# Performance work log

Measured on AMD Instinct MI355X. Metric: run time of the kernel, lower is better.

Reference implementation:

```python
import jax, jax.numpy as jnp
import numpy as np

B, T, D, H, W = 2, 16, 64, 64, 64
MAX_GROWTH = 0.0  # max_growth_rate init kwarg

def _ln(x, g, b):
    m = x.mean(-1, keepdims=True)
    v = x.var(-1, keepdims=True)
    return (x - m) * jax.lax.rsqrt(v + 1e-5) * g + b

def _pscan(A, X):
    # linear recurrence h_t = A_t*h_{t-1} + X_t via Blelchlo-style associative scan over axis 1
    def comb(l, r):
        a1, x1 = l
        a2, x2 = r
        return a1 * a2, a2 * x1 + x2
    return jax.lax.associative_scan(comb, (A, X), axis=1)[1]

def setup_inputs() -> dict:
    key = jax.random.key(0)
    ks = jax.random.split(key, 20)
    n = lambda k, s, sc=1.0: jax.random.normal(k, s, dtype=jnp.float32) * sc
    inp = dict(
        x_re=n(ks[0], (B, T, D, H, W)), x_im=n(ks[1], (B, T, D, H, W)),
        h_re=n(ks[2], (B * H * W, 1, D)), h_im=n(ks[3], (B * H * W, 1, D)),
        flux_re=n(ks[4], (B, D)), flux_im=n(ks[5], (B, D)),
        dt_seq=0.01 + 0.1 * jax.random.uniform(ks[6], (B, T), dtype=jnp.float32),
        g_s=jnp.ones(2 * D, jnp.float32), b_s=jnp.zeros(2 * D, jnp.float32),
        Wc=n(ks[7], (3, 3, 2 * D, 2 * D), 1.0 / np.sqrt(9 * 2 * D)), bc=jnp.zeros(2 * D, jnp.float32),
        g_t=jnp.ones(2 * D, jnp.float32), b_t=jnp.zeros(2 * D, jnp.float32),
        E_re=n(ks[8], (D, D), 1.0 / np.sqrt(D)), E_im=n(ks[9], (D, D), 1.0 / np.sqrt(D)),
        Dec_re=n(ks[10], (D, D), 1.0 / np.sqrt(D)), Dec_im=n(ks[11], (D, D), 1.0 / np.sqrt(D)),
        lam_flux_raw=jnp.zeros(D, jnp.float32),
        Wsrc_re=n(ks[12], (D, D), 1.0 / np.sqrt(D)), Wsrc_im=n(ks[13], (D, D), 1.0 / np.sqrt(D)),
        w_gate=n(ks[14], (D,)), b_gate=jnp.zeros(D, jnp.float32),
        lam_re_raw=jnp.ones(D, jnp.float32), lam_im=n(ks[15], (D,)),
        W1=n(ks[16], (2 * D, 8 * D), 1.0 / np.sqrt(2 * D)), b1=jnp.zeros(8 * D, jnp.float32),
        W2=n(ks[17], (8 * D, 2 * D), 1.0 / np.sqrt(8 * D)), b2=jnp.zeros(2 * D, jnp.float32),
    )
    return inp

def _forward(x_re, x_im, h_re, h_im, flux_re, flux_im, dt_seq, g_s, b_s, Wc, bc, g_t, b_t,
             E_re, E_im, Dec_re, Dec_im, lam_flux_raw, Wsrc_re, Wsrc_im, w_gate, b_gate,
             lam_re_raw, lam_im, W1, b1, W2, b2):
    # channel-last complex field (B,T,H,W,D)
    x = jnp.moveaxis(x_re, 2, -1) + 1j * jnp.moveaxis(x_im, 2, -1)
    # --- spatial residual branch: LN -> Clifford(= real 2D conv on [re;im] channels) ---
    xr = jnp.concatenate([x.real, x.imag], -1)  # (B,T,H,W,2D)
    xn = _ln(xr, g_s, b_s).reshape(B * T, H, W, 2 * D)
    xs = jax.lax.conv_general_dilated(xn, Wc, (1, 1), 'SAME',
                                      dimension_numbers=('NHWC', 'HWIO', 'NHWC')) + bc
    xs = xs.reshape(B, T, H, W, 2 * D)
    x = x + (xs[..., :D] + 1j * xs[..., D:])
    # --- eigen-basis encode ---
    x_eig = jnp.einsum('bthwd,de->bthwe', x, E_re + 1j * E_im)
    x_mean = x_eig.mean((2, 3))  # (B,T,D)
    # --- flux tracker scan ---
    lam_f = jax.nn.softplus(lam_flux_raw)
    A_flux = jnp.exp(-lam_f * dt_seq[..., None])  # (B,T,D) real decay
    flux = _pscan(A_flux.astype(x_mean.dtype), x_mean * dt_seq[..., None])
    flux = flux + (flux_re + 1j * flux_im)[:, None, :] * jnp.cumprod(A_flux, axis=1)
    source = jnp.einsum('btd,de->bte', flux, Wsrc_re + 1j * Wsrc_im)
    gate = jax.nn.sigmoid(flux.real * w_gate + b_gate)  # real gate in [0,1]
    flux_out = flux[:, -1]
    ge = gate[:, :, None, None, :]
    forcing = x_eig * ge + source[:, :, None, None, :] * (1.0 - ge)
    # --- temporal propagator (exact exponential integrator) ---
    lam = (MAX_GROWTH - jax.nn.softplus(lam_re_raw)) + 1j * lam_im  # Re(lam) <= max_growth_rate
    op_decay = jnp.exp(lam * dt_seq[..., None])            # (B,T,D)
    op_forcing = (op_decay - 1.0) / lam
    u = forcing * op_forcing[:, :, None, None, :]          # (B,T,H,W,D)
    h_prev = (h_re + 1j * h_im).reshape(B, H, W, D)
    u = u.at[:, 0].add(h_prev * op_decay[:, 0][:, None, None, :])
    A_full = jnp.broadcast_to(op_decay[:, :, None, None, :], u.shape)
    u_out = _pscan(A_full, u)                              # (B,T,H,W,D)
    h_out = u_out[:, -1].reshape(B * H * W, 1, D)
    # --- decode + temporal LN/FFN residual ---
    decoded = jnp.einsum('bthwd,de->bthwe', u_out, Dec_re + 1j * Dec_im)
    dn = _ln(jnp.concatenate([decoded.real, decoded.imag], -1), g_t, b_t)
    h1 = jax.nn.gelu(jnp.einsum('bthwc,cf->bthwf', dn, W1) + b1)
    d2 = jnp.einsum('bthwf,fc->bthwc', h1, W2) + b2
    delta = d2[..., :D] + 1j * d2[..., D:]
    z = x + decoded + delta
    return z, h_out, flux_out

def reference(x_re, x_im, h_re, h_im, flux_re, flux_im, dt_seq, g_s, b_s, Wc, bc, g_t, b_t,
              E_re, E_im, Dec_re, Dec_im, lam_flux_raw, Wsrc_re, Wsrc_im, w_gate, b_gate,
              lam_re_raw, lam_im, W1, b1, W2, b2):
    z, h_out, flux_out = _forward(x_re, x_im, h_re, h_im, flux_re, flux_im, dt_seq, g_s, b_s,
                                  Wc, bc, g_t, b_t, E_re, E_im, Dec_re, Dec_im, lam_flux_raw,
                                  Wsrc_re, Wsrc_im, w_gate, b_gate, lam_re_raw, lam_im,
                                  W1, b1, W2, b2)
    # complex outputs returned as real/imag stacked on last axis
    return (jnp.stack([z.real, z.imag], -1),
            jnp.stack([h_out.real, h_out.imag], -1),
            jnp.stack([flux_out.real, flux_out.imag], -1))
```

## Files before the change

kernel.cpp:

```cpp
#include <hip/hip_runtime.h>
#include <hip/hip_bf16.h>


typedef __hip_bfloat16 bf16;
typedef __attribute__((ext_vector_type(8))) short bhalf8;
typedef __attribute__((ext_vector_type(4))) float floatx4;

#define DEV __device__ __forceinline__

DEV float b2f(const bf16 x) { return __bfloat162float(x); }
DEV bf16  f2b(float x)      { return __float2bfloat16(x); }
DEV unsigned short f2bu(float x) { bf16 h = f2b(x); return *(unsigned short*)&h; }
DEV float bu2f(unsigned short u) { unsigned int t = ((unsigned int)u) << 16; return *(float*)&t; }
DEV float softplusf(float x){ return x > 20.f ? x : log1pf(expf(x)); }
DEV float geluf(float x) {
    float v = x * fmaf(x * x, 0.10294324f, 2.30220819f);
    float e = __builtin_amdgcn_exp2f(-v);
    return x * __builtin_amdgcn_rcpf(1.f + e);
}

static constexpr int B_ = 2, T_ = 16, D_ = 64, HW = 4096;
static constexpr int NPIX = B_ * T_ * HW;
static constexpr long long N1 = (long long)NPIX * 128;

static constexpr long long BUFA  = 0;
static constexpr long long XUBF  = N1;
static constexpr long long DECBF = N1 + N1 / 2;
static constexpr long long XNBF  = 2 * N1;
static constexpr long long XCBF  = 2 * N1 + N1 / 2;
static constexpr long long XMEAN = 3 * N1;
static constexpr long long TABS  = XMEAN + 4096;
static constexpr long long FLAGO = TABS + 14336;
static constexpr long long WCP   = FLAGO + 64;
static constexpr long long W1P   = WCP + 73728;
static constexpr long long W2P   = W1P + 32768;
static constexpr long long WEP   = W2P + 32768;
static constexpr long long WDP   = WEP + 8192;

static constexpr long long ZOUT = 0;
static constexpr long long HOUT = 16777216;
static constexpr long long FOUT = 17825792;

DEV float ld(const void* p, long long i, bool bf) {
    if (bf) return b2f(((const bf16*)p)[i]);
    return ((const float*)p)[i];
}

__global__ void k_detect(const unsigned short* __restrict__ x, float* __restrict__ ws) {
    int lane = threadIdx.x;
    int cnt = 0;
    for (int i = lane; i < 256; i += 64) {
        int e = (x[i] >> 7) & 0xFF;
        cnt += (e >= 100 && e <= 140) ? 1 : 0;
    }
    for (int m = 1; m < 64; m <<= 1) cnt += __shfl_xor(cnt, m, 64);
    if (lane == 0) ws[FLAGO] = (cnt >= 224) ? 1.f : 0.f;
}

__global__ void k_convert(const void* Wc, const void* W1, const void* W2,
                          const void* Er, const void* Ei, const void* Dr, const void* Di,
                          float* ws) {
    bool bf = ws[FLAGO] != 0.f;
    int i = blockIdx.x * 256 + threadIdx.x;
    unsigned short* wcp = (unsigned short*)(ws + WCP);
    unsigned short* w1p = (unsigned short*)(ws + W1P);
    unsigned short* w2p = (unsigned short*)(ws + W2P);
    unsigned short* wep = (unsigned short*)(ws + WEP);
    unsigned short* wdp = (unsigned short*)(ws + WDP);
    if (i < 147456) {
        int j = i & 7, lane = (i >> 3) & 63, nt = (i >> 9) & 7, kc = (i >> 12) & 3, tap = i >> 14;
        int ic = kc * 32 + ((lane >> 4) << 3) + j, oc = nt * 16 + (lane & 15);
        wcp[i] = f2bu(ld(Wc, tap * 16384 + ic * 128 + oc, bf)); return;
    } i -= 147456;
    if (i < 65536) {
        int j = i & 7, lane = (i >> 3) & 63, nt = (i >> 9) & 31, kc = i >> 14;
        int ic = kc * 32 + ((lane >> 4) << 3) + j, oc = nt * 16 + (lane & 15);
        w1p[i] = f2bu(ld(W1, ic * 512 + oc, bf)); return;
    } i -= 65536;
    if (i < 65536) {
        int j = i & 7, lane = (i >> 3) & 63, nt = (i >> 9) & 7, kc = i >> 12;
        int ic = kc * 32 + ((lane >> 4) << 3) + j, oc = nt * 16 + (lane & 15);
        w2p[i] = f2bu(ld(W2, ic * 128 + oc, bf)); return;
    } i -= 65536;
    if (i < 16384) {
        int j = i & 7, lane = (i >> 3) & 63, nt = (i >> 9) & 7, kc = i >> 12;
        int k = kc * 32 + ((lane >> 4) << 3) + j, n = nt * 16 + (lane & 15);
        float v;
        if (k < 64) v = (n < 64) ? ld(Er, k * 64 + n, bf) : ld(Ei, k * 64 + (n - 64), bf);
        else        v = (n < 64) ? -ld(Ei, (k - 64) * 64 + n, bf) : ld(Er, (k - 64) * 64 + (n - 64), bf);
        wep[i] = f2bu(v); return;
    } i -= 16384;
    if (i < 16384) {
        int j = i & 7, lane = (i >> 3) & 63, nt = (i >> 9) & 7, kc = i >> 12;
        int k = kc * 32 + ((lane >> 4) << 3) + j, n = nt * 16 + (lane & 15);
        float v;
        if (k < 64) v = (n < 64) ? ld(Dr, k * 64 + n, bf) : ld(Di, k * 64 + (n - 64), bf);
        else        v = (n < 64) ? -ld(Di, (k - 64) * 64 + n, bf) : ld(Dr, (k - 64) * 64 + (n - 64), bf);
        wdp[i] = f2bu(v); return;
    }
}

__global__ __launch_bounds__(256) void kA_ln(const void* __restrict__ xre,
                                             const void* __restrict__ xim,
                                             const void* __restrict__ gs,
                                             const void* __restrict__ bs,
                                             float* __restrict__ ws) {
    __shared__ unsigned short sr[64][72] __attribute__((aligned(16)));
    __shared__ unsigned short si[64][72] __attribute__((aligned(16)));
    __shared__ float red[2][4][64];
    __shared__ float mv[64], rv[64], gb[256];
    bool bf = ws[FLAGO] != 0.f;
    int blk = blockIdx.x;
    int bt = blk >> 6;
    int px0 = (blk & 63) * 64;
    int tid = threadIdx.x;
    gb[tid] = (tid < 128) ? ld(gs, tid, bf) : ld(bs, tid - 128, bf);
    if (bf) {
        const unsigned short* xr16 = (const unsigned short*)xre;
        const unsigned short* xi16 = (const unsigned short*)xim;
        for (int l = tid; l < 1024; l += 256) {
            int a = l >> 9, dd = (l >> 3) & 63, ck = l & 7;
            long long src = (long long)bt * 262144 + (long long)dd * 4096 + px0 + ck * 8;
            bhalf8 v = *(const bhalf8*)&(a ? xi16 : xr16)[src];
            *(bhalf8*)&(a ? si : sr)[dd][ck * 8] = v;
        }
    } else {
        for (int l = tid; l < 8192; l += 256) {
            int a = l >> 12, dd = (l >> 6) & 63, px = l & 63;
            float v = ((const float*)(a ? xim : xre))[(long long)bt * 262144 + (long long)dd * 4096 + px0 + px];
            (a ? si : sr)[dd][px] = f2bu(v);
        }
    }
    __syncthreads();
    int px = tid & 63, part = tid >> 6;
    float s = 0.f, ss = 0.f;
    for (int d = part * 16; d < part * 16 + 16; d++) {
        float r = bu2f(sr[d][px]), q = bu2f(si[d][px]);
        s += r + q; ss += r * r + q * q;
    }
    red[0][part][px] = s; red[1][part][px] = ss;
    __syncthreads();
    if (tid < 64) {
        float S  = red[0][0][tid] + red[0][1][tid] + red[0][2][tid] + red[0][3][tid];
        float SS = red[1][0][tid] + red[1][1][tid] + red[1][2][tid] + red[1][3][tid];
        float m = S * (1.f / 128.f);
        mv[tid] = m;
        rv[tid] = rsqrtf(SS * (1.f / 128.f) - m * m + 1e-5f);
    }
    __syncthreads();
    unsigned short* xcb = (unsigned short*)(ws + XCBF);
    unsigned short* xnb = (unsigned short*)(ws + XNBF);
    long long pbase = ((long long)bt * 4096 + px0) * 128;
    for (int l = tid; l < 8192; l += 256) {
        int p2 = l >> 7, ch = l & 127, d = ch & 63;
        unsigned short raw = (ch < 64 ? sr : si)[d][p2];
        float v = bu2f(raw);
        xcb[pbase + p2 * 128 + ch] = raw;
        xnb[pbase + p2 * 128 + ch] = f2bu((v - mv[p2]) * rv[p2] * gb[ch] + gb[128 + ch]);
    }
}

__global__ __launch_bounds__(256) void kB_conv(const void* __restrict__ bc,
                                               float* __restrict__ ws) {
    __shared__ unsigned short xt[3][64][136] __attribute__((aligned(16)));
    bool bf = ws[FLAGO] != 0.f;
    int blk = blockIdx.x, bt = blk >> 6, h = blk & 63;
    int tid = threadIdx.x, lane = tid & 63, wv = tid >> 6;
    int m16 = lane & 15, quad = lane >> 4;
    const unsigned short* xnb = (const unsigned short*)(ws + XNBF);
    const unsigned short* wcp = (const unsigned short*)(ws + WCP);
    bhalf8 zero8 = {0, 0, 0, 0, 0, 0, 0, 0};
    for (int l = tid; l < 3072; l += 256) {
        int r = l >> 10, rem = l & 1023, col = rem >> 4, ck = rem & 15;
        int hr = h - 1 + r;
        bhalf8 v = zero8;
        if (hr >= 0 && hr < 64)
            v = *(const bhalf8*)&xnb[(((long long)bt * 4096 + hr * 64 + col) << 7) + ck * 8];
        *(bhalf8*)&xt[r][col][ck * 8] = v;
    }
    __syncthreads();
    floatx4 acc[4][2];
    #pragma unroll
    for (int mt = 0; mt < 4; mt++)
        #pragma unroll
        for (int nt = 0; nt < 2; nt++)
            acc[mt][nt] = (floatx4){0.f, 0.f, 0.f, 0.f};
    for (int tap = 0; tap < 9; tap++) {
        int dy = tap / 3, dx = tap - dy * 3;
        #pragma unroll
        for (int kc = 0; kc < 4; kc++) {
            bhalf8 bfr[2];
            #pragma unroll
            for (int nt = 0; nt < 2; nt++)
                bfr[nt] = *(const bhalf8*)&wcp[((((tap * 4 + kc) * 8) + (wv * 2 + nt)) * 64 + lane) * 8];
            #pragma unroll
            for (int mt = 0; mt < 4; mt++) {
                int col = mt * 16 + m16 + dx - 1;
                bhalf8 af = zero8;
                if (col >= 0 && col < 64)
                    af = *(const bhalf8*)&xt[dy][col][kc * 32 + quad * 8];
                acc[mt][0] = __builtin_amdgcn_mfma_f32_16x16x32_bf16(af, bfr[0], acc[mt][0], 0, 0, 0);
                acc[mt][1] = __builtin_amdgcn_mfma_f32_16x16x32_bf16(af, bfr[1], acc[mt][1], 0, 0, 0);
            }
        }
    }
    __syncthreads();
    unsigned short (*At)[136] = (unsigned short(*)[136])&xt[0][0][0];
    const unsigned short* xcb = (const unsigned short*)(ws + XCBF);
    unsigned short* xub = (unsigned short*)(ws + XUBF);
    #pragma unroll
    for (int nt = 0; nt < 2; nt++) {
        int n = wv * 32 + nt * 16 + m16;
        float bcv = ld(bc, n, bf);
        #pragma unroll
        for (int mt = 0; mt < 4; mt++)
            #pragma unroll
            for (int r = 0; r < 4; r++) {
                int m = mt * 16 + quad * 4 + r;
                long long p = (long long)bt * 4096 + h * 64 + m;
                unsigned short u = f2bu(acc[mt][nt][r] + bu2f(xcb[p * 128 + n]) + bcv);
                xub[p * 128 + n] = u;
                At[m][n] = u;
            }
    }
    __syncthreads();
    const unsigned short* wep = (const unsigned short*)(ws + WEP);
    long long px0 = (long long)blk * 64;
    floatx4 acce[4][2];
    #pragma unroll
    for (int mt = 0; mt < 4; mt++)
        #pragma unroll
        for (int nt = 0; nt < 2; nt++)
            acce[mt][nt] = (floatx4){0.f, 0.f, 0.f, 0.f};
    #pragma unroll
    for (int kc = 0; kc < 4; kc++) {
        bhalf8 bfr[2];
        #pragma unroll
        for (int nt = 0; nt < 2; nt++)
            bfr[nt] = *(const bhalf8*)&wep[(((kc * 8) + wv * 2 + nt) * 64 + lane) * 8];
        #pragma unroll
        for (int mt = 0; mt < 4; mt++) {
            bhalf8 af = *(const bhalf8*)&At[mt * 16 + m16][kc * 32 + quad * 8];
            acce[mt][0] = __builtin_amdgcn_mfma_f32_16x16x32_bf16(af, bfr[0], acce[mt][0], 0, 0, 0);
            acce[mt][1] = __builtin_amdgcn_mfma_f32_16x16x32_bf16(af, bfr[1], acce[mt][1], 0, 0, 0);
        }
    }
    unsigned short* xeb = (unsigned short*)(ws + BUFA);
    #pragma unroll
    for (int nt = 0; nt < 2; nt++) {
        int n = wv * 32 + nt * 16 + m16;
        float part = 0.f;
        #pragma unroll
        for (int mt = 0; mt < 4; mt++)
            #pragma unroll
            for (int r = 0; r < 4; r++) {
                int m = mt * 16 + quad * 4 + r;
                xeb[(px0 + m) * 128 + n] = f2bu(acce[mt][nt][r]);
                part += acce[mt][nt][r];
            }
        part += __shfl_xor(part, 16, 64);
        part += __shfl_xor(part, 32, 64);
        if (quad == 0) atomicAdd(ws + XMEAN + bt * 128 + n, part);
    }
}

__global__ __launch_bounds__(256) void kD_flux(const void* __restrict__ fxr, const void* __restrict__ fxi,
                                               const void* __restrict__ dtseq, const void* __restrict__ lamflux,
                                               const void* __restrict__ Wsr, const void* __restrict__ Wsi,
                                               const void* __restrict__ wgate, const void* __restrict__ bgate,
                                               const void* __restrict__ lamreraw, const void* __restrict__ lamim,
                                               float* __restrict__ ws, void* __restrict__ outv) {
    bool bfo = ws[FLAGO] != 0.f;
    int b = blockIdx.x;
    int tid = threadIdx.x;
    int d = tid & 63, g = tid >> 6;
    __shared__ float fr[64], fi[64], psr[4][64], psi[4][64];
    float lam_f = softplusf(ld(lamflux, d, bfo));
    float lre = -softplusf(ld(lamreraw, d, bfo));
    float lim = ld(lamim, d, bfo);
    float cr = 0.f, ci = 0.f;
    if (g == 0) { cr = ld(fxr, b * 64 + d, bfo); ci = ld(fxi, b * 64 + d, bfo); }
    float* tabs = ws + TABS;
    const float* xmean = ws + XMEAN;
    for (int t = 0; t < 16; t++) {
        float dt = ld(dtseq, b * 16 + t, bfo);
        int idx = b * 1024 + t * 64 + d;
        if (g == 0) {
            float A = expf(-lam_f * dt);
            float xr = xmean[(b * 16 + t) * 128 + d]      * (1.f / 4096.f) * dt;
            float xq = xmean[(b * 16 + t) * 128 + 64 + d] * (1.f / 4096.f) * dt;
            cr = A * cr + xr; ci = A * ci + xq;
            fr[d] = cr; fi[d] = ci;
        }
        __syncthreads();
        {
            float pr = 0.f, pi = 0.f;
            #pragma unroll
            for (int k = 0; k < 16; k++) {
                int d2 = g * 16 + k;
                float wr = ld(Wsr, d2 * 64 + d, bfo), wi = ld(Wsi, d2 * 64 + d, bfo);
                pr += fr[d2] * wr - fi[d2] * wi;
                pi += fr[d2] * wi + fi[d2] * wr;
            }
            psr[g][d] = pr; psi[g][d] = pi;
        }
        if (g == 1) {
            float od  = expf(lre * dt);
            float odr = od * cosf(lim * dt);
            float odi = od * sinf(lim * dt);
            tabs[3 * 2048 + idx] = odr; tabs[4 * 2048 + idx] = odi;
            float den = lre * lre + lim * lim;
            float tr = odr - 1.f;
            tabs[5 * 2048 + idx] = (tr * lre + odi * lim) / den;
            tabs[6 * 2048 + idx] = (odi * lre - tr * lim) / den;
        }
        __syncthreads();
        if (g == 0) {
            float sr = psr[0][d] + psr[1][d] + psr[2][d] + psr[3][d];
            float si2 = psi[0][d] + psi[1][d] + psi[2][d] + psi[3][d];
            tabs[1 * 2048 + idx] = sr; tabs[2 * 2048 + idx] = si2;
            tabs[0 * 2048 + idx] = 1.f / (1.f + expf(-(cr * ld(wgate, d, bfo) + ld(bgate, d, bfo))));
            if (t == 15) {
                if (bfo) {
                    bf16* ob = (bf16*)outv;
                    ob[FOUT + (b * 64 + d) * 2]     = f2b(cr);
                    ob[FOUT + (b * 64 + d) * 2 + 1] = f2b(ci);
                } else {
                    float* of = (float*)outv;
                    of[FOUT + (b * 64 + d) * 2]     = cr;
                    of[FOUT + (b * 64 + d) * 2 + 1] = ci;
                }
            }
        }
    }
}

__global__ __launch_bounds__(256) void kE_scan(const void* __restrict__ hre,
                                               const void* __restrict__ him,
                                               float* __restrict__ ws, void* __restrict__ outv) {
    __shared__ float tab[7][16][64];
    bool bfo = ws[FLAGO] != 0.f;
    int tid = threadIdx.x;
    long long G = (long long)blockIdx.x * 256 + tid;
    int d0 = (int)(G & 31) * 2;
    int pixg = (int)(G >> 5);
    int pix = pixg & 4095;
    int b = pixg >> 12;
    const float* tabs = ws + TABS;
    for (int l = tid; l < 7 * 1024; l += 256) {
        int a = l >> 10, idx = l & 1023;
        ((float*)tab)[l] = tabs[a * 2048 + b * 1024 + idx];
    }
    __syncthreads();
    long long hidx = ((long long)b * 4096 + pix) * 64 + d0;
    float cr0, ci0, cr1, ci1;
    if (bfo) {
        unsigned int r2 = *(const unsigned int*)&((const unsigned short*)hre)[hidx];
        unsigned int i2 = *(const unsigned int*)&((const unsigned short*)him)[hidx];
        cr0 = bu2f((unsigned short)(r2 & 0xffff)); cr1 = bu2f((unsigned short)(r2 >> 16));
        ci0 = bu2f((unsigned short)(i2 & 0xffff)); ci1 = bu2f((unsigned short)(i2 >> 16));
    } else {
        float2 r2 = *(const float2*)((const float*)hre + hidx);
        float2 i2 = *(const float2*)((const float*)him + hidx);
        cr0 = r2.x; cr1 = r2.y; ci0 = i2.x; ci1 = i2.y;
    }
    const unsigned short* xe = (const unsigned short*)(ws + BUFA);
    unsigned short* ub = (unsigned short*)(ws + XCBF);
    for (int t = 0; t < 16; t++) {
        long long base = ((long long)((b * 16 + t) * 4096 + pix)) * 128 + d0;
        unsigned int xr2 = *(const unsigned int*)&xe[base];
        unsigned int xi2 = *(const unsigned int*)&xe[base + 64];
        float2 gt2  = *(const float2*)&tab[0][t][d0];
        float2 sr2  = *(const float2*)&tab[1][t][d0];
        float2 si2  = *(const float2*)&tab[2][t][d0];
        float2 odr2 = *(const float2*)&tab[3][t][d0];
        float2 odi2 = *(const float2*)&tab[4][t][d0];
        float2 ofr2 = *(const float2*)&tab[5][t][d0];
        float2 ofi2 = *(const float2*)&tab[6][t][d0];
        {
            float xr = bu2f((unsigned short)(xr2 & 0xffff));
            float xi = bu2f((unsigned short)(xi2 & 0xffff));
            float fre = xr * gt2.x + sr2.x * (1.f - gt2.x);
            float fim = xi * gt2.x + si2.x * (1.f - gt2.x);
            float ure = fre * ofr2.x - fim * ofi2.x;
            float uim = fre * ofi2.x + fim * ofr2.x;
            float n0 = odr2.x * cr0 - odi2.x * ci0 + ure;
            float n1 = odr2.x * ci0 + odi2.x * cr0 + uim;
            cr0 = n0; ci0 = n1;
        }
        {
            float xr = bu2f((unsigned short)(xr2 >> 16));
            float xi = bu2f((unsigned short)(xi2 >> 16));
            float fre = xr * gt2.y + sr2.y * (1.f - gt2.y);
            float fim = xi * gt2.y + si2.y * (1.f - gt2.y);
            float ure = fre * ofr2.y - fim * ofi2.y;
            float uim = fre * ofi2.y + fim * ofr2.y;
            float n0 = odr2.y * cr1 - odi2.y * ci1 + ure;
            float n1 = odr2.y * ci1 + odi2.y * cr1 + uim;
            cr1 = n0; ci1 = n1;
        }
        *(unsigned int*)&ub[base]      = (unsigned int)f2bu(cr0) | ((unsigned int)f2bu(cr1) << 16);
        *(unsigned int*)&ub[base + 64] = (unsigned int)f2bu(ci0) | ((unsigned int)f2bu(ci1) << 16);
    }
    if (bfo) {
        uint2 hv;
        hv.x = (unsigned int)f2bu(cr0) | ((unsigned int)f2bu(ci0) << 16);
        hv.y = (unsigned int)f2bu(cr1) | ((unsigned int)f2bu(ci1) << 16);
        *(uint2*)((unsigned short*)outv + HOUT + 2 * hidx) = hv;
    } else {
        float4 hv; hv.x = cr0; hv.y = ci0; hv.z = cr1; hv.w = ci1;
        *(float4*)((float*)outv + HOUT + 2 * hidx) = hv;
    }
}

__global__ __launch_bounds__(256, 4) void kMLP(const void* __restrict__ gt_,
                                               const void* __restrict__ bt_,
                                               const void* __restrict__ b1v,
                                               const void* __restrict__ b2v,
                                               float* __restrict__ ws, void* __restrict__ outv) {
    __shared__ unsigned char POOL[16384] __attribute__((aligned(16)));
    __shared__ unsigned short Dt[32][136] __attribute__((aligned(16)));
    __shared__ unsigned short A1[32][136] __attribute__((aligned(16)));
    __shared__ float gbt[256];
    __shared__ float gb2[128];
    __shared__ float psS[4][32], psQ[4][32];
    __shared__ float mvv[32], rvv[32];
    unsigned short (*UA)[136] = (unsigned short(*)[136])POOL;
    unsigned short (*h1f)[2][64][8] = (unsigned short(*)[2][64][8])POOL;
    bool bf = ws[FLAGO] != 0.f;
    long long px0 = (long long)blockIdx.x * 32;
    int tid = threadIdx.x, lane = tid & 63, wv = tid >> 6;
    int m16 = lane & 15, quad = lane >> 4;
    gbt[tid] = (tid < 128) ? ld(gt_, tid, bf) : ld(bt_, tid - 128, bf);
    if (tid < 128) gb2[tid] = ld(b2v, tid, bf);
    const unsigned short* uo = (const unsigned short*)(ws + XCBF);
    for (int l = tid; l < 512; l += 256) {
        int p2 = l >> 4, ck = l & 15;
        *(bhalf8*)&UA[p2][ck * 8] = *(const bhalf8*)&uo[(px0 + p2) * 128 + ck * 8];
    }
    __syncthreads();
    const unsigned short* wdp = (const unsigned short*)(ws + WDP);
    floatx4 accd[2][2];
    #pragma unroll
    for (int mt = 0; mt < 2; mt++)
        #pragma unroll
        for (int nt = 0; nt < 2; nt++)
            accd[mt][nt] = (floatx4){0.f, 0.f, 0.f, 0.f};
    #pragma unroll
    for (int kc = 0; kc < 4; kc++) {
        bhalf8 bfr0 = *(const bhalf8*)&wdp[(((kc * 8) + wv * 2 + 0) * 64 + lane) * 8];
        bhalf8 bfr1 = *(const bhalf8*)&wdp[(((kc * 8) + wv * 2 + 1) * 64 + lane) * 8];
        bhalf8 af0 = *(const bhalf8*)&UA[m16][kc * 32 + quad * 8];
        bhalf8 af1 = *(const bhalf8*)&UA[16 + m16][kc * 32 + quad * 8];
        accd[0][0] = __builtin_amdgcn_mfma_f32_16x16x32_bf16(af0, bfr0, accd[0][0], 0, 0, 0);
        accd[0][1] = __builtin_amdgcn_mfma_f32_16x16x32_bf16(af0, bfr1, accd[0][1], 0, 0, 0);
        accd[1][0] = __builtin_amdgcn_mfma_f32_16x16x32_bf16(af1, bfr0, accd[1][0], 0, 0, 0);
        accd[1][1] = __builtin_amdgcn_mfma_f32_16x16x32_bf16(af1, bfr1, accd[1][1], 0, 0, 0);
    }
    #pragma unroll
    for (int mt = 0; mt < 2; mt++)
        #pragma unroll
        for (int r = 0; r < 4; r++) {
            int mrow = mt * 16 + quad * 4 + r;
            float a0 = accd[mt][0][r], a1 = accd[mt][1][r];
            Dt[mrow][wv * 32 + m16]      = f2bu(a0);
            Dt[mrow][wv * 32 + 16 + m16] = f2bu(a1);
            float s = a0 + a1, q = a0 * a0 + a1 * a1;
            #pragma unroll
            for (int msk = 1; msk <= 8; msk <<= 1) {
                s += __shfl_xor(s, msk, 64);
                q += __shfl_xor(q, msk, 64);
            }
            if (m16 == 0) { psS[wv][mrow] = s; psQ[wv][mrow] = q; }
        }
    __syncthreads();
    if (tid < 32) {
        float S = psS[0][tid] + psS[1][tid] + psS[2][tid] + psS[3][tid];
        float Q = psQ[0][tid] + psQ[1][tid] + psQ[2][tid] + psQ[3][tid];
        float m = S * (1.f / 128.f);
        mvv[tid] = m;
        rvv[tid] = rsqrtf(Q * (1.f / 128.f) - m * m + 1e-5f);
    }
    __syncthreads();
    #pragma unroll
    for (int mt = 0; mt < 2; mt++)
        #pragma unroll
        for (int r = 0; r < 4; r++) {
            int mrow = mt * 16 + quad * 4 + r;
            float mu = mvv[mrow], rs = rvv[mrow];
            #pragma unroll
            for (int nt = 0; nt < 2; nt++) {
                int n = wv * 32 + nt * 16 + m16;
                A1[mrow][n] = f2bu((accd[mt][nt][r] - mu) * rs * gbt[n] + gbt[128 + n]);
            }
        }
    __syncthreads();
    const unsigned short* w1p = (const unsigned short*)(ws + W1P);
    const unsigned short* w2p = (const unsigned short*)(ws + W2P);
    floatx4 acc2[2][2];
    #pragma unroll
    for (int mt = 0; mt < 2; mt++)
        #pragma unroll
        for (int nt = 0; nt < 2; nt++)
            acc2[mt][nt] = (floatx4){0.f, 0.f, 0.f, 0.f};
    #pragma unroll
    for (int ph = 0; ph < 2; ph++) {
        floatx4 acc1[2][4];
        #pragma unroll
        for (int mt = 0; mt < 2; mt++)
            #pragma unroll
            for (int nt4 = 0; nt4 < 4; nt4++)
                acc1[mt][nt4] = (floatx4){0.f, 0.f, 0.f, 0.f};
        #pragma unroll
        for (int kc = 0; kc < 4; kc++) {
            bhalf8 af0 = *(const bhalf8*)&A1[m16][kc * 32 + quad * 8];
            bhalf8 af1 = *(const bhalf8*)&A1[16 + m16][kc * 32 + quad * 8];
            #pragma unroll
            for (int nt4 = 0; nt4 < 4; nt4++) {
                int nt = ph * 4 + nt4;
                bhalf8 bfr = *(const bhalf8*)&w1p[(((kc * 32) + wv * 8 + nt) * 64 + lane) * 8];
                acc1[0][nt4] = __builtin_amdgcn_mfma_f32_16x16x32_bf16(af0, bfr, acc1[0][nt4], 0, 0, 0);
                acc1[1][nt4] = __builtin_amdgcn_mfma_f32_16x16x32_bf16(af1, bfr, acc1[1][nt4], 0, 0, 0);
            }
        }
        if (ph == 0) __syncthreads();
        #pragma unroll
        for (int nt4 = 0; nt4 < 4; nt4++) {
            int nt = ph * 4 + nt4;
            int n = (wv * 8 + nt) * 16 + m16;
            float b1f = ld(b1v, n, bf);
            int qp = ((nt * 2) + (m16 >> 3)) & 3;
            int slot = wv * 2 + (nt4 >> 1);
            int j = m16 & 7;
            #pragma unroll
            for (int mt = 0; mt < 2; mt++)
                #pragma unroll
                for (int r = 0; r < 4; r++)
                    h1f[slot][mt][qp * 16 + quad * 4 + r][j] =
                        f2bu(geluf(acc1[mt][nt4][r] + b1f));
        }
        __syncthreads();
        #pragma unroll
        for (int s = 0; s < 8; s++) {
            int kc2g = (s >> 1) * 4 + (s & 1) + ph * 2;
            bhalf8 a0 = *(const bhalf8*)&h1f[s][0][lane][0];
            bhalf8 a1 = *(const bhalf8*)&h1f[s][1][lane][0];
            #pragma unroll
            for (int nt = 0; nt < 2; nt++) {
                bhalf8 bfr = *(const bhalf8*)&w2p[(((kc2g * 8) + wv * 2 + nt) * 64 + lane) * 8];
                acc2[0][nt] = __builtin_amdgcn_mfma_f32_16x16x32_bf16(a0, bfr, acc2[0][nt], 0, 0, 0);
                acc2[1][nt] = __builtin_amdgcn_mfma_f32_16x16x32_bf16(a1, bfr, acc2[1][nt], 0, 0, 0);
            }
        }
        if (ph == 0) __syncthreads();
    }
    #pragma unroll
    for (int nt = 0; nt < 2; nt++) {
        int n = wv * 32 + nt * 16 + m16;
        #pragma unroll
        for (int mt = 0; mt < 2; mt++)
            #pragma unroll
            for (int r = 0; r < 4; r++)
                A1[mt * 16 + quad * 4 + r][n] = f2bu(acc2[mt][nt][r]);
    }
    __syncthreads();
    {
        const unsigned short* xub = (const unsigned short*)(ws + XUBF);
        int pxl = tid >> 3, dc = (tid & 7) * 8;
        long long p = px0 + pxl;
        bhalf8 cre = *(const bhalf8*)&A1[pxl][dc];
        bhalf8 cim = *(const bhalf8*)&A1[pxl][64 + dc];
        bhalf8 xr8 = *(const bhalf8*)&xub[p * 128 + dc];
        bhalf8 xi8 = *(const bhalf8*)&xub[p * 128 + 64 + dc];
        bhalf8 dr8 = *(const bhalf8*)&Dt[pxl][dc];
        bhalf8 di8 = *(const bhalf8*)&Dt[pxl][64 + dc];
        float zr[8], zi[8];
        #pragma unroll
        for (int k = 0; k < 8; k++) {
            zr[k] = bu2f((unsigned short)cre[k]) + gb2[dc + k]
                  + bu2f((unsigned short)xr8[k]) + bu2f((unsigned short)dr8[k]);
            zi[k] = bu2f((unsigned short)cim[k]) + gb2[64 + dc + k]
                  + bu2f((unsigned short)xi8[k]) + bu2f((unsigned short)di8[k]);
        }
        if (bf) {
            unsigned short o[16];
            #pragma unroll
            for (int k = 0; k < 8; k++) { o[2 * k] = f2bu(zr[k]); o[2 * k + 1] = f2bu(zi[k]); }
            unsigned short* ob = (unsigned short*)outv;
            *(bhalf8*)&ob[ZOUT + p * 128 + 2 * dc]     = *(bhalf8*)&o[0];
            *(bhalf8*)&ob[ZOUT + p * 128 + 2 * dc + 8] = *(bhalf8*)&o[8];
        } else {
            float* of = (float*)outv + ZOUT + p * 128 + 2 * dc;
            #pragma unroll
            for (int k = 0; k < 8; k++) { of[2 * k] = zr[k]; of[2 * k + 1] = zi[k]; }
        }
    }
}

extern "C" void kernel_launch(void* const* d_in, const int* in_sizes, int n_in,
                              void* d_out, int out_size, void* d_ws, size_t ws_size,
                              hipStream_t stream) {
    const void* x_re  = d_in[0];
    const void* x_im  = d_in[1];
    const void* h_re  = d_in[2];
    const void* h_im  = d_in[3];
    const void* fl_re = d_in[4];
    const void* fl_im = d_in[5];
    const void* dtseq = d_in[6];
    const void* g_s   = d_in[7];
    const void* b_s   = d_in[8];
    const void* Wc    = d_in[9];
    const void* bc    = d_in[10];
    const void* g_t   = d_in[11];
    const void* b_t   = d_in[12];
    const void* E_re  = d_in[13];
    const void* E_im  = d_in[14];
    const void* De_re = d_in[15];
    const void* De_im = d_in[16];
    const void* lamfl = d_in[17];
    const void* Ws_re = d_in[18];
    const void* Ws_im = d_in[19];
    const void* wgate = d_in[20];
    const void* bgate = d_in[21];
    const void* lamrr = d_in[22];
    const void* lamim = d_in[23];
    const void* W1    = d_in[24];
    const void* b1    = d_in[25];
    const void* W2    = d_in[26];
    const void* b2    = d_in[27];
    float* ws = (float*)d_ws;

    hipMemsetAsync((char*)d_ws + XMEAN * sizeof(float), 0, 4096 * sizeof(float), stream);
    k_detect<<<1, 64, 0, stream>>>((const unsigned short*)x_re, ws);
    k_convert<<<1216, 256, 0, stream>>>(Wc, W1, W2, E_re, E_im, De_re, De_im, ws);
    kA_ln<<<2048, 256, 0, stream>>>(x_re, x_im, g_s, b_s, ws);
    kB_conv<<<2048, 256, 0, stream>>>(bc, ws);
    kD_flux<<<2, 256, 0, stream>>>(fl_re, fl_im, dtseq, lamfl, Ws_re, Ws_im,
                                   wgate, bgate, lamrr, lamim, ws, d_out);
    kE_scan<<<1024, 256, 0, stream>>>(h_re, h_im, ws, d_out);
    kMLP<<<4096, 256, 0, stream>>>(g_t, b_t, b1, b2, ws, d_out);
}
```

Baseline: 414.9 us.

## Split decay tables out of flux kernel, pack LN stores, fold decoded into MLP accumulator

Moves the per-(b,t,d) decay and integral table computation from the serial flux kernel into a separate parallel kernel. The flux kernel now stages the source weights in shared memory and hoists the gate loads out of the time loop. The LN kernel writes two bf16 channels per 32-bit store. The MLP kernel drops its Dt shared buffer, adds the decoded accumulators straight into the output accumulator, removes one barrier and raises the occupancy hint from 4 to 5. Dropping that barrier and keeping accd live across the MLP loop add risk of a shared-memory race and of higher register pressure.

```diff
diff --git a/kernel.cpp b/kernel.cpp
--- a/kernel.cpp
+++ b/kernel.cpp
@@ -100,6 +100,29 @@
     }
 }
 
+__global__ void kD_tabs(const void* __restrict__ dtseq,
+                        const void* __restrict__ lamreraw,
+                        const void* __restrict__ lamim,
+                        float* __restrict__ ws) {
+    bool bfo = ws[FLAGO] != 0.f;
+    int idx = blockIdx.x * 256 + threadIdx.x;
+    if (idx >= 2048) return;
+    int d = idx & 63, t = (idx >> 6) & 15, b = idx >> 10;
+    float dt = ld(dtseq, b * 16 + t, bfo);
+    float lre = -softplusf(ld(lamreraw, d, bfo));
+    float lim = ld(lamim, d, bfo);
+    float od  = expf(lre * dt);
+    float odr = od * cosf(lim * dt);
+    float odi = od * sinf(lim * dt);
+    float* tabs = ws + TABS;
+    int i2 = b * 1024 + t * 64 + d;
+    tabs[3 * 2048 + i2] = odr; tabs[4 * 2048 + i2] = odi;
+    float den = lre * lre + lim * lim;
+    float tr = odr - 1.f;
+    tabs[5 * 2048 + i2] = (tr * lre + odi * lim) / den;
+    tabs[6 * 2048 + i2] = (odi * lre - tr * lim) / den;
+}
+
 __global__ __launch_bounds__(256) void kA_ln(const void* __restrict__ xre,
                                              const void* __restrict__ xim,
                                              const void* __restrict__ gs,
@@ -151,12 +174,18 @@
     unsigned short* xcb = (unsigned short*)(ws + XCBF);
     unsigned short* xnb = (unsigned short*)(ws + XNBF);
     long long pbase = ((long long)bt * 4096 + px0) * 128;
-    for (int l = tid; l < 8192; l += 256) {
-        int p2 = l >> 7, ch = l & 127, d = ch & 63;
-        unsigned short raw = (ch < 64 ? sr : si)[d][p2];
-        float v = bu2f(raw);
-        xcb[pbase + p2 * 128 + ch] = raw;
-        xnb[pbase + p2 * 128 + ch] = f2bu((v - mv[p2]) * rv[p2] * gb[ch] + gb[128 + ch]);
+    for (int l = tid; l < 4096; l += 256) {
+        int p2 = l >> 6, ch2 = (l & 63) * 2;
+        int d0 = ch2 & 63;
+        unsigned short raw0 = (ch2 < 64 ? sr : si)[d0][p2];
+        unsigned short raw1 = (ch2 < 64 ? sr : si)[d0 + 1][p2];
+        float v0 = bu2f(raw0), v1 = bu2f(raw1);
+        unsigned int cpk = (unsigned int)raw0 | ((unsigned int)raw1 << 16);
+        unsigned short n0 = f2bu((v0 - mv[p2]) * rv[p2] * gb[ch2]     + gb[128 + ch2]);
+        unsigned short n1 = f2bu((v1 - mv[p2]) * rv[p2] * gb[ch2 + 1] + gb[129 + ch2]);
+        unsigned int npk = (unsigned int)n0 | ((unsigned int)n1 << 16);
+        *(unsigned int*)&xcb[pbase + p2 * 128 + ch2] = cpk;
+        *(unsigned int*)&xnb[pbase + p2 * 128 + ch2] = npk;
     }
 }
 
@@ -268,16 +297,19 @@
                                                const void* __restrict__ dtseq, const void* __restrict__ lamflux,
                                                const void* __restrict__ Wsr, const void* __restrict__ Wsi,
                                                const void* __restrict__ wgate, const void* __restrict__ bgate,
-                                               const void* __restrict__ lamreraw, const void* __restrict__ lamim,
                                                float* __restrict__ ws, void* __restrict__ outv) {
     bool bfo = ws[FLAGO] != 0.f;
     int b = blockIdx.x;
     int tid = threadIdx.x;
     int d = tid & 63, g = tid >> 6;
     __shared__ float fr[64], fi[64], psr[4][64], psi[4][64];
+    __shared__ float Wr[64][64], Wi[64][64];
+    for (int l = tid; l < 4096; l += 256) {
+        Wr[l >> 6][l & 63] = ld(Wsr, l, bfo);
+        Wi[l >> 6][l & 63] = ld(Wsi, l, bfo);
+    }
     float lam_f = softplusf(ld(lamflux, d, bfo));
-    float lre = -softplusf(ld(lamreraw, d, bfo));
-    float lim = ld(lamim, d, bfo);
+    float wg = ld(wgate, d, bfo), bg = ld(bgate, d, bfo);
     float cr = 0.f, ci = 0.f;
     if (g == 0) { cr = ld(fxr, b * 64 + d, bfo); ci = ld(fxi, b * 64 + d, bfo); }
     float* tabs = ws + TABS;
@@ -298,28 +330,18 @@
             #pragma unroll
             for (int k = 0; k < 16; k++) {
                 int d2 = g * 16 + k;
-                float wr = ld(Wsr, d2 * 64 + d, bfo), wi = ld(Wsi, d2 * 64 + d, bfo);
+                float wr = Wr[d2][d], wi = Wi[d2][d];
                 pr += fr[d2] * wr - fi[d2] * wi;
                 pi += fr[d2] * wi + fi[d2] * wr;
             }
             psr[g][d] = pr; psi[g][d] = pi;
-        }
-        if (g == 1) {
-            float od  = expf(lre * dt);
-            float odr = od * cosf(lim * dt);
-            float odi = od * sinf(lim * dt);
-            tabs[3 * 2048 + idx] = odr; tabs[4 * 2048 + idx] = odi;
-            float den = lre * lre + lim * lim;
-            float tr = odr - 1.f;
-            tabs[5 * 2048 + idx] = (tr * lre + odi * lim) / den;
-            tabs[6 * 2048 + idx] = (odi * lre - tr * lim) / den;
         }
         __syncthreads();
         if (g == 0) {
             float sr = psr[0][d] + psr[1][d] + psr[2][d] + psr[3][d];
             float si2 = psi[0][d] + psi[1][d] + psi[2][d] + psi[3][d];
             tabs[1 * 2048 + idx] = sr; tabs[2 * 2048 + idx] = si2;
-            tabs[0 * 2048 + idx] = 1.f / (1.f + expf(-(cr * ld(wgate, d, bfo) + ld(bgate, d, bfo))));
+            tabs[0 * 2048 + idx] = 1.f / (1.f + expf(-(cr * wg + bg)));
             if (t == 15) {
                 if (bfo) {
                     bf16* ob = (bf16*)outv;
@@ -413,13 +435,12 @@
     }
 }
 
-__global__ __launch_bounds__(256, 4) void kMLP(const void* __restrict__ gt_,
+__global__ __launch_bounds__(256, 5) void kMLP(const void* __restrict__ gt_,
                                                const void* __restrict__ bt_,
                                                const void* __restrict__ b1v,
                                                const void* __restrict__ b2v,
                                                float* __restrict__ ws, void* __restrict__ outv) {
     __shared__ unsigned char POOL[16384] __attribute__((aligned(16)));
-    __shared__ unsigned short Dt[32][136] __attribute__((aligned(16)));
     __shared__ unsigned short A1[32][136] __attribute__((aligned(16)));
     __shared__ float gbt[256];
     __shared__ float gb2[128];
@@ -463,8 +484,6 @@
         for (int r = 0; r < 4; r++) {
             int mrow = mt * 16 + quad * 4 + r;
             float a0 = accd[mt][0][r], a1 = accd[mt][1][r];
-            Dt[mrow][wv * 32 + m16]      = f2bu(a0);
-            Dt[mrow][wv * 32 + 16 + m16] = f2bu(a1);
             float s = a0 + a1, q = a0 * a0 + a1 * a1;
             #pragma unroll
             for (int msk = 1; msk <= 8; msk <<= 1) {
@@ -523,7 +542,6 @@
                 acc1[1][nt4] = __builtin_amdgcn_mfma_f32_16x16x32_bf16(af1, bfr, acc1[1][nt4], 0, 0, 0);
             }
         }
-        if (ph == 0) __syncthreads();
         #pragma unroll
         for (int nt4 = 0; nt4 < 4; nt4++) {
             int nt = ph * 4 + nt4;
@@ -561,7 +579,7 @@
         for (int mt = 0; mt < 2; mt++)
             #pragma unroll
             for (int r = 0; r < 4; r++)
-                A1[mt * 16 + quad * 4 + r][n] = f2bu(acc2[mt][nt][r]);
+                A1[mt * 16 + quad * 4 + r][n] = f2bu(acc2[mt][nt][r] + accd[mt][nt][r]);
     }
     __syncthreads();
     {
@@ -572,15 +590,11 @@
         bhalf8 cim = *(const bhalf8*)&A1[pxl][64 + dc];
         bhalf8 xr8 = *(const bhalf8*)&xub[p * 128 + dc];
         bhalf8 xi8 = *(const bhalf8*)&xub[p * 128 + 64 + dc];
-        bhalf8 dr8 = *(const bhalf8*)&Dt[pxl][dc];
-        bhalf8 di8 = *(const bhalf8*)&Dt[pxl][64 + dc];
         float zr[8], zi[8];
         #pragma unroll
         for (int k = 0; k < 8; k++) {
-            zr[k] = bu2f((unsigned short)cre[k]) + gb2[dc + k]
-                  + bu2f((unsigned short)xr8[k]) + bu2f((unsigned short)dr8[k]);
-            zi[k] = bu2f((unsigned short)cim[k]) + gb2[64 + dc + k]
-                  + bu2f((unsigned short)xi8[k]) + bu2f((unsigned short)di8[k]);
+            zr[k] = bu2f((unsigned short)cre[k]) + gb2[dc + k] + bu2f((unsigned short)xr8[k]);
+            zi[k] = bu2f((unsigned short)cim[k]) + gb2[64 + dc + k] + bu2f((unsigned short)xi8[k]);
         }
         if (bf) {
             unsigned short o[16];
@@ -633,10 +647,11 @@
     hipMemsetAsync((char*)d_ws + XMEAN * sizeof(float), 0, 4096 * sizeof(float), stream);
     k_detect<<<1, 64, 0, stream>>>((const unsigned short*)x_re, ws);
     k_convert<<<1216, 256, 0, stream>>>(Wc, W1, W2, E_re, E_im, De_re, De_im, ws);
+    kD_tabs<<<8, 256, 0, stream>>>(dtseq, lamrr, lamim, ws);
     kA_ln<<<2048, 256, 0, stream>>>(x_re, x_im, g_s, b_s, ws);
     kB_conv<<<2048, 256, 0, stream>>>(bc, ws);
     kD_flux<<<2, 256, 0, stream>>>(fl_re, fl_im, dtseq, lamfl, Ws_re, Ws_im,
-                                   wgate, bgate, lamrr, lamim, ws, d_out);
+                                   wgate, bgate, ws, d_out);
     kE_scan<<<1024, 256, 0, stream>>>(h_re, h_im, ws, d_out);
     kMLP<<<4096, 256, 0, stream>>>(g_t, b_t, b1, b2, ws, d_out);
 }
```

Measured after the change: 421.9 us. No clear change (+1.7%).
